# Kernel optimization log

Measured on AMD Instinct MI355X. Metric: run time of the kernel, lower is better.

## Reference

```python
import jax, jax.numpy as jnp
import numpy as np

EPS = 1e-5

def ln(x, gamma, beta):
    m = jnp.mean(x, axis=-1, keepdims=True)
    std = jnp.sqrt(jnp.var(x, axis=-1, keepdims=True) + EPS)
    return gamma * ((x - m) / (std + EPS)) + beta

def hard_sigmoid(x):
    return jnp.clip(0.2 * x + 0.5, 0.0, 1.0)

def setup_inputs() -> dict:
    key = jax.random.key(0)
    B, T, D, U, UEP = 64, 2048, 256, 256, 64
    ks = jax.random.split(key, 16)
    def gn(k, shape, s=0.05):
        return (jax.random.normal(k, shape, dtype=jnp.float32) * s)
    inp = {}
    inp['x'] = jax.random.normal(ks[0], (B, T, D), dtype=jnp.float32)
    inp['mask'] = jax.random.randint(ks[1], (B, T), 0, 2, dtype=jnp.int32)
    inp['W'] = gn(ks[2], (D, 3 * U))
    inp['U'] = gn(ks[3], (U, 3 * U))
    inp['b'] = jnp.zeros((3 * U,), jnp.float32)
    inp['gammas'] = 1.0 + gn(ks[4], (2, 3 * U), 0.1)
    inp['betas'] = gn(ks[5], (2, 3 * U), 0.1)
    inp['W_EP'] = gn(ks[6], (D, 3 * UEP))
    inp['U_EP'] = gn(ks[7], (UEP, 3 * UEP))
    inp['b_EP'] = jnp.zeros((3 * UEP,), jnp.float32)
    inp['gammas_EP'] = 1.0 + gn(ks[8], (2, 3 * UEP), 0.1)
    inp['betas_EP'] = gn(ks[9], (2, 3 * UEP), 0.1)
    inp['W1_EP'] = gn(ks[10], (UEP, 1))
    inp['b1_EP'] = jnp.zeros((1,), jnp.float32)
    return inp

def _gru_step(s1, h_tm1, Umat, g1, bt1, dim):
    # s1: precomputed ln(x@W + b)  [B, 3*dim]
    s2 = ln(h_tm1 @ Umat[:, :2 * dim], g1[:2 * dim], bt1[:2 * dim])
    s = hard_sigmoid(s1[:, :2 * dim] + s2)
    z, r = s[:, :dim], s[:, dim:2 * dim]
    hh = ln((r * h_tm1) @ Umat[:, 2 * dim:], g1[2 * dim:], bt1[2 * dim:])
    return z * h_tm1 + (1.0 - z) * jnp.tanh(s1[:, 2 * dim:] + hh)

def _encoder(x, mask, W, U, b, gammas, betas, W_EP, U_EP, b_EP, gammas_EP, betas_EP, W1_EP, b1_EP):
    B, T, D = x.shape
    dim = U.shape[0]
    dim_ep = U_EP.shape[0]
    # input projections + their LayerNorms depend only on x -> precompute (same math)
    s1_all = ln(jnp.einsum('btd,dk->btk', x, W) + b, gammas[0], betas[0])          # [B,T,3U]
    s1_ep_all = ln(jnp.einsum('btd,dk->btk', x, W_EP) + b_EP, gammas_EP[0], betas_EP[0])  # [B,T,3Uep]
    s1_all = jnp.swapaxes(s1_all, 0, 1)        # [T,B,3U]
    s1_ep_all = jnp.swapaxes(s1_ep_all, 0, 1)  # [T,B,3Uep]
    xm_all = (mask > 0).T                      # [T,B] bool

    def step(carry, inp):
        h_tm1, hep_tm1, is_end_tm1 = carry
        s1, s1e, xm = inp
        h_tm1 = jnp.where(is_end_tm1[:, None] > 0.5, 0.0, h_tm1)
        h = _gru_step(s1, h_tm1, U, gammas[1], betas[1], dim)
        h = jnp.where(xm[:, None], h, h_tm1)
        hep = _gru_step(s1e, hep_tm1, U_EP, gammas_EP[1], betas_EP[1], dim_ep)
        hep = jnp.where(xm[:, None], hep, hep_tm1)
        is_end = jnp.round(jax.nn.sigmoid(hep_tm1 @ W1_EP + b1_EP))[:, 0]
        return (h, hep, is_end), (h, is_end)

    init = (jnp.zeros((B, dim), x.dtype), jnp.zeros((B, dim_ep), x.dtype), jnp.zeros((B,), x.dtype))
    _, (h_seq, end_seq) = jax.lax.scan(step, init, (s1_all, s1_ep_all, xm_all))
    return jnp.swapaxes(h_seq, 0, 1), jnp.swapaxes(end_seq, 0, 1)  # [B,T,U], [B,T]

def reference(x, mask, W, U, b, gammas, betas, W_EP, U_EP, b_EP, gammas_EP, betas_EP, W1_EP, b1_EP):
    return _encoder(x, mask, W, U, b, gammas, betas, W_EP, U_EP, b_EP, gammas_EP, betas_EP, W1_EP, b1_EP)
```

## Files before the change

### kernel.cpp

```cpp
#include <hip/hip_runtime.h>


typedef _Float16 h2  __attribute__((ext_vector_type(2)));
typedef _Float16 v8h __attribute__((ext_vector_type(8)));

__device__ __forceinline__ float fdot2_(h2 a, h2 b, float c) {
#if __has_builtin(__builtin_amdgcn_fdot2)
  return __builtin_amdgcn_fdot2(a, b, c, false);
#else
  return c + (float)a[0] * (float)b[0] + (float)a[1] * (float)b[1];
#endif
}

template <int I>
__device__ __forceinline__ h2 pr(v8h v) {
  h2 r; r[0] = v[2 * I]; r[1] = v[2 * I + 1]; return r;
}

__device__ __forceinline__ void wg_barrier() {
  __builtin_amdgcn_sched_barrier(0);
  asm volatile("s_waitcnt lgkmcnt(0)" ::: "memory");
  __builtin_amdgcn_sched_barrier(0);
  __builtin_amdgcn_s_barrier();
  __builtin_amdgcn_sched_barrier(0);
}

__global__ __launch_bounds__(256) void prep_kernel(
    const float* __restrict__ W, const float* __restrict__ U,
    const float* __restrict__ W_EP,
    _Float16* __restrict__ wt, _Float16* __restrict__ uzr,
    _Float16* __restrict__ uh, float* __restrict__ wept)
{
  const int blk = blockIdx.x;
  const int k = threadIdx.x;
  if (blk < 768) {
    const int j = blk;
    wt[(size_t)j * 256 + k] = (_Float16)W[(size_t)k * 768 + j];
  } else if (blk < 1280) {
    const int j = blk - 768;
    uzr[(size_t)j * 256 + k] = (_Float16)U[(size_t)k * 768 + j];
  } else if (blk < 1536) {
    const int j = blk - 1280;
    const int p = k >> 3, e = k & 7;
    uh[((size_t)p * 256 + j) * 8 + e] = (_Float16)U[(size_t)k * 768 + 512 + j];
  } else {
    const int j = blk - 1536;
    wept[(size_t)j * 256 + k] = W_EP[(size_t)k * 192 + j];
  }
}

__global__ __launch_bounds__(256) void ph1_main_kernel(
    const float* __restrict__ x, const _Float16* __restrict__ wt,
    const float* __restrict__ bvec, const float* __restrict__ gam,
    const float* __restrict__ bet, _Float16* __restrict__ s1out)
{
  __shared__ __align__(16) _Float16 xs[16][256];
  __shared__ float sp[16][768];
  const int tid = threadIdx.x;
  const size_t row0 = (size_t)blockIdx.x * 16;

  #pragma unroll
  for (int i = 0; i < 16; ++i)
    xs[i][tid] = (_Float16)x[(row0 + i) * 256 + tid];
  __syncthreads();

  #pragma unroll 1
  for (int cc = 0; cc < 3; ++cc) {
    const int col = cc * 256 + tid;
    const v8h* wp = (const v8h*)(wt + (size_t)col * 256);
    float acc[16];
    #pragma unroll
    for (int r = 0; r < 16; ++r) acc[r] = 0.f;
    #pragma unroll 4
    for (int c = 0; c < 32; ++c) {
      const v8h w8 = wp[c];
      #pragma unroll
      for (int r = 0; r < 16; ++r) {
        const v8h x8 = *(const v8h*)(&xs[r][c * 8]);
        acc[r] = fdot2_(pr<0>(x8), pr<0>(w8), acc[r]);
        acc[r] = fdot2_(pr<1>(x8), pr<1>(w8), acc[r]);
        acc[r] = fdot2_(pr<2>(x8), pr<2>(w8), acc[r]);
        acc[r] = fdot2_(pr<3>(x8), pr<3>(w8), acc[r]);
      }
    }
    const float bb = bvec[col];
    #pragma unroll
    for (int r = 0; r < 16; ++r) sp[r][col] = acc[r] + bb;
  }
  __syncthreads();

  const int w = tid >> 6, lane = tid & 63;
  for (int rr = 0; rr < 4; ++rr) {
    const int r = (w << 2) | rr;
    float vals[12], sum = 0.f, sq = 0.f;
    #pragma unroll
    for (int j = 0; j < 12; ++j) {
      const float v = sp[r][lane + (j << 6)];
      vals[j] = v; sum += v; sq += v * v;
    }
    #pragma unroll
    for (int m = 32; m >= 1; m >>= 1) {
      sum += __shfl_xor(sum, m); sq += __shfl_xor(sq, m);
    }
    const float mean = sum * (1.f / 768.f);
    const float var = sq * (1.f / 768.f) - mean * mean;
    const float inv = 1.f / (sqrtf(var + 1e-5f) + 1e-5f);
    #pragma unroll
    for (int j = 0; j < 12; ++j) {
      const int c = lane + (j << 6);
      s1out[(row0 + r) * 768 + c] =
          (_Float16)(gam[c] * ((vals[j] - mean) * inv) + bet[c]);
    }
  }
}

__global__ __launch_bounds__(192) void ph1_ep_kernel(
    const float* __restrict__ x, const float* __restrict__ wept,
    const float* __restrict__ bvec, const float* __restrict__ gam,
    const float* __restrict__ bet, void* __restrict__ s1e, const int store64)
{
  __shared__ __align__(16) float xs[16][256];
  __shared__ double sp[16][192];
  const int tid = threadIdx.x;
  const size_t row0 = (size_t)blockIdx.x * 16;

  for (int idx = tid; idx < 4096; idx += 192)
    xs[idx >> 8][idx & 255] = x[row0 * 256 + idx];
  __syncthreads();

  {
    const float4* wp = (const float4*)(wept + (size_t)tid * 256);
    double acc[16];
    #pragma unroll
    for (int r = 0; r < 16; ++r) acc[r] = 0.0;
    #pragma unroll 2
    for (int c = 0; c < 64; ++c) {
      const float4 w4 = wp[c];
      #pragma unroll
      for (int r = 0; r < 16; ++r) {
        const float4 x4 = *(const float4*)(&xs[r][c * 4]);
        acc[r] += (double)x4.x * (double)w4.x;
        acc[r] += (double)x4.y * (double)w4.y;
        acc[r] += (double)x4.z * (double)w4.z;
        acc[r] += (double)x4.w * (double)w4.w;
      }
    }
    const double bb = (double)bvec[tid];
    #pragma unroll
    for (int r = 0; r < 16; ++r) sp[r][tid] = acc[r] + bb;
  }
  __syncthreads();

  const int w = tid >> 6, lane = tid & 63;
  for (int r = w; r < 16; r += 3) {
    double vals[3], sum = 0.0, sq = 0.0;
    #pragma unroll
    for (int j = 0; j < 3; ++j) {
      const double v = sp[r][lane + (j << 6)];
      vals[j] = v; sum += v; sq += v * v;
    }
    #pragma unroll
    for (int m = 32; m >= 1; m >>= 1) {
      sum += __shfl_xor(sum, m); sq += __shfl_xor(sq, m);
    }
    const double mean = sum * (1.0 / 192.0);
    const double var = sq * (1.0 / 192.0) - mean * mean;
    const double den = sqrt(var + 1e-5) + 1e-5;
    #pragma unroll
    for (int j = 0; j < 3; ++j) {
      const int c = lane + (j << 6);
      const double vv = (double)gam[c] * ((vals[j] - mean) / den) + (double)bet[c];
      if (store64) ((double*)s1e)[(row0 + r) * 192 + c] = vv;
      else         ((float*)s1e)[(row0 + r) * 192 + c] = (float)vv;
    }
  }
}

#define OFF_UH     0
#define OFF_MASK   131072
#define OFF_HEP    139264
#define OFF_ZEE    139776
#define OFF_RHEP   140288
#define OFF_EPZRP  140800
#define OFF_EPHHP  140928
#define OFF_H2     140992
#define OFF_RH     141504
#define OFF_HF     142016
#define OFF_Z      143040
#define OFF_ZRP    144064
#define OFF_HHP    144128
#define OFF_FLAG   144160
#define SCAN_LDS_BYTES 144192

__global__ __launch_bounds__(512, 2) void scan_kernel(
    const _Float16* __restrict__ uzr_g, const _Float16* __restrict__ uh_g,
    const float* __restrict__ U_EP, const _Float16* __restrict__ s1,
    const void* __restrict__ s1e_v, const int s1e64,
    const int* __restrict__ mask,
    const float* __restrict__ gam1, const float* __restrict__ bet1,
    const float* __restrict__ gamep1, const float* __restrict__ betep1,
    const float* __restrict__ W1, const float* __restrict__ b1,
    float* __restrict__ out)
{
  extern __shared__ char sm[];
  const int t = threadIdx.x;
  const int b = blockIdx.x;
  const int w = t >> 6;
  const int je  = t >> 2;
  const int qe  = t & 3;
  const int jeh = (t & 255) >> 2;

  float*  hf    = (float*)(sm + OFF_HF);
  float*  flagp = (float*)(sm + OFF_FLAG);
  double* hepd  = (double*)(sm + OFF_HEP);
  int*    maskl = (int*)(sm + OFF_MASK);

  {
    const v8h* src = (const v8h*)uh_g;
    v8h* dst = (v8h*)(sm + OFF_UH);
    #pragma unroll
    for (int i = 0; i < 16; ++i) dst[i * 512 + t] = src[i * 512 + t];
  }
  #pragma unroll
  for (int i = 0; i < 4; ++i) maskl[i * 512 + t] = mask[((size_t)b << 11) + i * 512 + t];

  v8h uzrv[32];
  {
    const v8h* up = (const v8h*)uzr_g + (size_t)t * 32;
    #pragma unroll
    for (int c = 0; c < 32; ++c) uzrv[c] = up[c];
  }
  float uez[16], ueh[16];
  #pragma unroll
  for (int i = 0; i < 16; ++i) uez[i] = U_EP[(size_t)(16 * qe + i) * 192 + je];
  #pragma unroll
  for (int i = 0; i < 16; ++i) ueh[i] = U_EP[(size_t)(16 * qe + i) * 192 + 128 + jeh];

  const float gz = gam1[t],                bz = bet1[t];
  const float gh = gam1[512 + (t & 255)],  bh = bet1[512 + (t & 255)];
  const float gse = gamep1[je],            bse = betep1[je];
  const float ghe = gamep1[128 + jeh],     bhe = betep1[128 + jeh];
  const double w1d = (double)W1[t & 63];
  const double b1d = (double)b1[0];
  const double* dptr = (const double*)s1e_v;
  const float*  fptr = (const float*)s1e_v;

  if (t < 128) { h2 z2; z2[0] = (_Float16)0.f; z2[1] = (_Float16)0.f;
                 ((h2*)(sm + OFF_H2))[t] = z2; }
  if (t < 256) hf[t] = 0.f;
  if (t < 64)  hepd[t] = 0.0;
  if (t < 2)   flagp[t] = 0.f;

  const size_t n0 = (size_t)b << 11;
  float  s1zr_c = (float)s1[n0 * 768 + t];
  float  s1h_c  = (float)s1[n0 * 768 + 512 + (t & 255)];
  double s1ezr_c = s1e64 ? dptr[n0 * 192 + je]
                         : (double)fptr[n0 * 192 + je];
  double s1ehh_c = s1e64 ? dptr[n0 * 192 + 128 + jeh]
                         : (double)fptr[n0 * 192 + 128 + jeh];
  __syncthreads();

  for (int tt = 0; tt < 2048; ++tt) {
    const size_t n = ((size_t)b << 11) | (size_t)tt;
    const float fz = (flagp[tt & 1] > 0.5f) ? 0.f : 1.f;

    if (tt > 0 && t < 256) out[(n - 1) * 256 + t] = hf[t];

    const int ttn = (tt < 2047) ? tt + 1 : 2047;
    const size_t np1 = ((size_t)b << 11) | (size_t)ttn;
    const float  s1zr_n = (float)s1[np1 * 768 + t];
    const float  s1h_n  = (float)s1[np1 * 768 + 512 + (t & 255)];
    const double s1ezr_n = s1e64 ? dptr[np1 * 192 + je]
                                 : (double)fptr[np1 * 192 + je];
    const double s1ehh_n = s1e64 ? dptr[np1 * 192 + 128 + jeh]
                                 : (double)fptr[np1 * 192 + 128 + jeh];

    if (w == 7) {
      double p = hepd[t & 63] * w1d;
      #pragma unroll
      for (int m = 1; m <= 32; m <<= 1) p += __shfl_xor(p, m);
      if (t == 448) {
        const float e = ((p + b1d) > 0.0) ? 1.f : 0.f;
        flagp[(tt + 1) & 1] = e;
        out[(size_t)33554432 + n] = e;
      }
    }

    float d;
    {
      const v8h* hv = (const v8h*)(sm + OFF_H2);
      float a0 = 0.f, a1 = 0.f, a2 = 0.f, a3 = 0.f;
      #pragma unroll
      for (int c = 0; c < 32; ++c) {
        const v8h hc = hv[c];
        a0 = fdot2_(pr<0>(hc), pr<0>(uzrv[c]), a0);
        a1 = fdot2_(pr<1>(hc), pr<1>(uzrv[c]), a1);
        a2 = fdot2_(pr<2>(hc), pr<2>(uzrv[c]), a2);
        a3 = fdot2_(pr<3>(hc), pr<3>(uzrv[c]), a3);
      }
      d = ((a0 + a1) + (a2 + a3)) * fz;
      float s_ = d, q_ = d * d;
      #pragma unroll
      for (int m = 1; m <= 32; m <<= 1) { s_ += __shfl_xor(s_, m); q_ += __shfl_xor(q_, m); }
      if ((t & 63) == 0) ((float2*)(sm + OFF_ZRP))[w] = make_float2(s_, q_);
    }
    double de;
    {
      const double2* hp = (const double2*)(hepd + 16 * qe);
      double acc = 0.0;
      #pragma unroll
      for (int i = 0; i < 8; ++i) {
        const double2 hv2 = hp[i];
        acc += hv2.x * (double)uez[2 * i] + hv2.y * (double)uez[2 * i + 1];
      }
      acc += __shfl_xor(acc, 1); acc += __shfl_xor(acc, 2);
      de = acc;
      double es = de, eq = de * de;
      #pragma unroll
      for (int m = 4; m <= 32; m <<= 1) { es += __shfl_xor(es, m); eq += __shfl_xor(eq, m); }
      if ((t & 63) == 0) ((double2*)(sm + OFF_EPZRP))[w] = make_double2(es, eq);
    }
    wg_barrier();

    {
      float S = 0.f, Q = 0.f;
      const float4* zp = (const float4*)(sm + OFF_ZRP);
      #pragma unroll
      for (int i = 0; i < 4; ++i) { const float4 v = zp[i]; S += v.x + v.z; Q += v.y + v.w; }
      const float mean = S * (1.f / 512.f);
      const float var = Q * (1.f / 512.f) - mean * mean;
      const float inv = 1.f / (sqrtf(var + 1e-5f) + 1e-5f);
      const float s2v = gz * ((d - mean) * inv) + bz;
      float sv = 0.2f * (s1zr_c + s2v) + 0.5f;
      sv = fminf(fmaxf(sv, 0.f), 1.f);
      if (t < 256) ((float*)(sm + OFF_Z))[t] = sv;
      else {
        const float rhv = sv * (fz * hf[t - 256]);
        ((_Float16*)(sm + OFF_RH))[t - 256] = (_Float16)rhv;
      }
    }
    if ((t & 3) == 0) {
      double S = 0.0, Q = 0.0;
      const double2* ep = (const double2*)(sm + OFF_EPZRP);
      #pragma unroll
      for (int i = 0; i < 8; ++i) { S += ep[i].x; Q += ep[i].y; }
      const double mean = S * (1.0 / 128.0);
      const double var = Q * (1.0 / 128.0) - mean * mean;
      const double den = sqrt(var + 1e-5) + 1e-5;
      const double s2e = (double)gse * ((de - mean) / den) + (double)bse;
      double se = 0.2 * (s1ezr_c + s2e) + 0.5;
      se = fmin(fmax(se, 0.0), 1.0);
      if (je < 64) ((double*)(sm + OFF_ZEE))[je] = se;
      else         ((double*)(sm + OFF_RHEP))[je - 64] = se * hepd[je - 64];
    }
    wg_barrier();

    float dh = 0.f;
    double deh = 0.0;
    if (t < 256) {
      const v8h* rhv8 = (const v8h*)(sm + OFF_RH);
      const v8h* uhv  = (const v8h*)(sm + OFF_UH);
      float c0 = 0.f, c1 = 0.f, c2 = 0.f, c3 = 0.f;
      #pragma unroll
      for (int p = 0; p < 32; ++p) {
        const v8h rc = rhv8[p];
        const v8h uc = uhv[p * 256 + t];
        c0 = fdot2_(pr<0>(rc), pr<0>(uc), c0);
        c1 = fdot2_(pr<1>(rc), pr<1>(uc), c1);
        c2 = fdot2_(pr<2>(rc), pr<2>(uc), c2);
        c3 = fdot2_(pr<3>(rc), pr<3>(uc), c3);
      }
      dh = (c0 + c1) + (c2 + c3);
      float s_ = dh, q_ = dh * dh;
      #pragma unroll
      for (int m = 1; m <= 32; m <<= 1) { s_ += __shfl_xor(s_, m); q_ += __shfl_xor(q_, m); }
      if ((t & 63) == 0) ((float2*)(sm + OFF_HHP))[w] = make_float2(s_, q_);
    } else {
      const double2* rp = (const double2*)((double*)(sm + OFF_RHEP) + 16 * qe);
      double acc = 0.0;
      #pragma unroll
      for (int i = 0; i < 8; ++i) {
        const double2 rv = rp[i];
        acc += rv.x * (double)ueh[2 * i] + rv.y * (double)ueh[2 * i + 1];
      }
      acc += __shfl_xor(acc, 1); acc += __shfl_xor(acc, 2);
      deh = acc;
      double es = deh, eq = deh * deh;
      #pragma unroll
      for (int m = 4; m <= 32; m <<= 1) { es += __shfl_xor(es, m); eq += __shfl_xor(eq, m); }
      if ((t & 63) == 0) ((double2*)(sm + OFF_EPHHP))[w - 4] = make_double2(es, eq);
    }
    wg_barrier();

    const int xm = maskl[tt];
    if (t < 256) {
      float S = 0.f, Q = 0.f;
      const float4* hp4 = (const float4*)(sm + OFF_HHP);
      #pragma unroll
      for (int i = 0; i < 2; ++i) { const float4 v = hp4[i]; S += v.x + v.z; Q += v.y + v.w; }
      const float mean = S * (1.f / 256.f);
      const float var = Q * (1.f / 256.f) - mean * mean;
      const float inv = 1.f / (sqrtf(var + 1e-5f) + 1e-5f);
      const float hhv = gh * ((dh - mean) * inv) + bh;
      const float z = ((float*)(sm + OFF_Z))[t];
      const float hzf = fz * hf[t];
      const float hn = z * hzf + (1.f - z) * tanhf(s1h_c + hhv);
      const float hc_ = (xm > 0) ? hn : hzf;
      hf[t] = hc_;
      const float ho = __shfl_xor(hc_, 1);
      if (!(t & 1)) {
        h2 p2; p2[0] = (_Float16)hc_; p2[1] = (_Float16)ho;
        ((h2*)(sm + OFF_H2))[t >> 1] = p2;
      }
    } else if ((t & 3) == 0) {
      double S = 0.0, Q = 0.0;
      const double2* ep = (const double2*)(sm + OFF_EPHHP);
      #pragma unroll
      for (int i = 0; i < 4; ++i) { S += ep[i].x; Q += ep[i].y; }
      const double mean = S * (1.0 / 64.0);
      const double var = Q * (1.0 / 64.0) - mean * mean;
      const double den = sqrt(var + 1e-5) + 1e-5;
      const double hhe = (double)ghe * ((deh - mean) / den) + (double)bhe;
      const double ze = ((double*)(sm + OFF_ZEE))[jeh];
      const double hold = hepd[jeh];
      const double hepn = ze * hold + (1.0 - ze) * tanh(s1ehh_c + hhe);
      hepd[jeh] = (xm > 0) ? hepn : hold;
    }
    wg_barrier();

    s1zr_c = s1zr_n; s1h_c = s1h_n; s1ezr_c = s1ezr_n; s1ehh_c = s1ehh_n;
  }
  if (t < 256) out[((((size_t)b << 11) | 2047)) * 256 + t] = hf[t];
}

extern "C" void kernel_launch(void* const* d_in, const int* in_sizes, int n_in,
                              void* d_out, int out_size, void* d_ws, size_t ws_size,
                              hipStream_t stream)
{
  (void)in_sizes; (void)n_in; (void)out_size;
  const float* x       = (const float*)d_in[0];
  const int*   mask    = (const int*)d_in[1];
  const float* W       = (const float*)d_in[2];
  const float* U       = (const float*)d_in[3];
  const float* bvec    = (const float*)d_in[4];
  const float* gammas  = (const float*)d_in[5];
  const float* betas   = (const float*)d_in[6];
  const float* W_EP    = (const float*)d_in[7];
  const float* U_EP    = (const float*)d_in[8];
  const float* b_EP    = (const float*)d_in[9];
  const float* gammasE = (const float*)d_in[10];
  const float* betasE  = (const float*)d_in[11];
  const float* W1_EP   = (const float*)d_in[12];
  const float* b1_EP   = (const float*)d_in[13];
  float* out = (float*)d_out;

  const size_t NR = 131072;
  const size_t S1_SZ    = NR * 768 * 2;
  const size_t S1E64_SZ = NR * 192 * 8;
  const size_t S1E32_SZ = NR * 192 * 4;
  const size_t WSMALL = 262144 + 131072 + 393216 + 196608;
  const int s1e64 = (ws_size >= S1_SZ + S1E64_SZ + WSMALL) ? 1 : 0;
  const size_t S1E_SZ = s1e64 ? S1E64_SZ : S1E32_SZ;
  if (ws_size < S1_SZ + S1E32_SZ + WSMALL) return;

  char* ws = (char*)d_ws;
  size_t off = 0;
  void* s1e      = (void*)(ws + off);      off += S1E_SZ;
  _Float16* s1   = (_Float16*)(ws + off);  off += S1_SZ;
  _Float16* uzr  = (_Float16*)(ws + off);  off += 262144;
  _Float16* uh   = (_Float16*)(ws + off);  off += 131072;
  _Float16* wt   = (_Float16*)(ws + off);  off += 393216;
  float* wept    = (float*)(ws + off);     off += 196608;

  prep_kernel<<<dim3(1728), dim3(256), 0, stream>>>(
      W, U, W_EP, wt, uzr, uh, wept);
  ph1_main_kernel<<<dim3(8192), dim3(256), 0, stream>>>(
      x, wt, bvec, gammas, betas, s1);
  ph1_ep_kernel<<<dim3(8192), dim3(192), 0, stream>>>(
      x, wept, b_EP, gammasE, betasE, s1e, s1e64);

  hipFuncSetAttribute(reinterpret_cast<const void*>(scan_kernel),
                      hipFuncAttributeMaxDynamicSharedMemorySize, SCAN_LDS_BYTES);
  scan_kernel<<<dim3(64), dim3(512), SCAN_LDS_BYTES, stream>>>(
      uzr, uh, U_EP, s1, (const void*)s1e, s1e64, mask,
      gammas + 768, betas + 768, gammasE + 192, betasE + 192,
      W1_EP, b1_EP, out);
}
```

Baseline: 20.75 ms.

## Split EP GRU recurrence into separate single-wave scan kernel feeding reset flags

```diff
diff --git a/kernel.cpp b/kernel.cpp
--- a/kernel.cpp
+++ b/kernel.cpp
@@ -15,6 +15,14 @@
 template <int I>
 __device__ __forceinline__ h2 pr(v8h v) {
   h2 r; r[0] = v[2 * I]; r[1] = v[2 * I + 1]; return r;
+}
+
+__device__ __forceinline__ double bcast_d(double v, int k) {
+  const int2 p = __builtin_bit_cast(int2, v);
+  int2 q;
+  q.x = __builtin_amdgcn_readlane(p.x, k);
+  q.y = __builtin_amdgcn_readlane(p.y, k);
+  return __builtin_bit_cast(double, q);
 }
 
 __device__ __forceinline__ void wg_barrier() {
@@ -38,7 +46,8 @@
     wt[(size_t)j * 256 + k] = (_Float16)W[(size_t)k * 768 + j];
   } else if (blk < 1280) {
     const int j = blk - 768;
-    uzr[(size_t)j * 256 + k] = (_Float16)U[(size_t)k * 768 + j];
+    const int c = k >> 3, e = k & 7;
+    uzr[((size_t)c * 512 + j) * 8 + e] = (_Float16)U[(size_t)k * 768 + j];
   } else if (blk < 1536) {
     const int j = blk - 1280;
     const int p = k >> 3, e = k & 7;
@@ -176,190 +185,211 @@
   }
 }
 
-#define OFF_UH     0
-#define OFF_MASK   131072
-#define OFF_HEP    139264
-#define OFF_ZEE    139776
-#define OFF_RHEP   140288
-#define OFF_EPZRP  140800
-#define OFF_EPHHP  140928
-#define OFF_H2     140992
-#define OFF_RH     141504
-#define OFF_HF     142016
-#define OFF_Z      143040
-#define OFF_ZRP    144064
-#define OFF_HHP    144128
-#define OFF_FLAG   144160
-#define SCAN_LDS_BYTES 144192
-
-__global__ __launch_bounds__(512, 2) void scan_kernel(
-    const _Float16* __restrict__ uzr_g, const _Float16* __restrict__ uh_g,
-    const float* __restrict__ U_EP, const _Float16* __restrict__ s1,
-    const void* __restrict__ s1e_v, const int s1e64,
-    const int* __restrict__ mask,
-    const float* __restrict__ gam1, const float* __restrict__ bet1,
+__global__ __launch_bounds__(64) void ep_scan_kernel(
+    const float* __restrict__ U_EP, const void* __restrict__ s1e_v,
+    const int s1e64, const int* __restrict__ mask,
     const float* __restrict__ gamep1, const float* __restrict__ betep1,
     const float* __restrict__ W1, const float* __restrict__ b1,
+    float* __restrict__ out, float* __restrict__ fzw)
+{
+  const int l = threadIdx.x;
+  const int b = blockIdx.x;
+
+  float uezA[64], uezB[64], uehh[64];
+  #pragma unroll
+  for (int k = 0; k < 64; ++k) uezA[k] = U_EP[(size_t)k * 192 + l];
+  #pragma unroll
+  for (int k = 0; k < 64; ++k) uezB[k] = U_EP[(size_t)k * 192 + 64 + l];
+  #pragma unroll
+  for (int k = 0; k < 64; ++k) uehh[k] = U_EP[(size_t)k * 192 + 128 + l];
+
+  const double gseA = (double)gamep1[l],       bseA = (double)betep1[l];
+  const double gseB = (double)gamep1[64 + l],  bseB = (double)betep1[64 + l];
+  const double ghe  = (double)gamep1[128 + l], bhe  = (double)betep1[128 + l];
+  const double w1d = (double)W1[l];
+  const double b1d = (double)b1[0];
+  const double* dptr = (const double*)s1e_v;
+  const float*  fptr = (const float*)s1e_v;
+
+  double hep = 0.0;
+  if (l == 0) fzw[(size_t)b * 2048] = 0.f;
+
+  const size_t n0 = (size_t)b << 11;
+  double s1eA_c = s1e64 ? dptr[n0 * 192 + l]       : (double)fptr[n0 * 192 + l];
+  double s1eB_c = s1e64 ? dptr[n0 * 192 + 64 + l]  : (double)fptr[n0 * 192 + 64 + l];
+  double s1eh_c = s1e64 ? dptr[n0 * 192 + 128 + l] : (double)fptr[n0 * 192 + 128 + l];
+  int mask_c = mask[n0];
+
+  for (int tt = 0; tt < 2048; ++tt) {
+    const size_t n = ((size_t)b << 11) | (size_t)tt;
+    const int ttn = (tt < 2047) ? tt + 1 : 2047;
+    const size_t np1 = ((size_t)b << 11) | (size_t)ttn;
+    const double s1eA_n = s1e64 ? dptr[np1 * 192 + l]       : (double)fptr[np1 * 192 + l];
+    const double s1eB_n = s1e64 ? dptr[np1 * 192 + 64 + l]  : (double)fptr[np1 * 192 + 64 + l];
+    const double s1eh_n = s1e64 ? dptr[np1 * 192 + 128 + l] : (double)fptr[np1 * 192 + 128 + l];
+    const int mask_n = mask[np1];
+
+    {
+      double p = hep * w1d;
+      #pragma unroll
+      for (int m = 1; m <= 32; m <<= 1) p += __shfl_xor(p, m);
+      if (l == 0) {
+        const float e = ((p + b1d) > 0.0) ? 1.f : 0.f;
+        if (tt < 2047) fzw[(size_t)b * 2048 + tt + 1] = e;
+        out[(size_t)33554432 + n] = e;
+      }
+    }
+
+    double dA = 0.0, dB = 0.0;
+    #pragma unroll
+    for (int k = 0; k < 64; ++k) {
+      const double hk = bcast_d(hep, k);
+      dA += hk * (double)uezA[k];
+      dB += hk * (double)uezB[k];
+    }
+    {
+      double S = dA + dB, Q = dA * dA + dB * dB;
+      #pragma unroll
+      for (int m = 1; m <= 32; m <<= 1) { S += __shfl_xor(S, m); Q += __shfl_xor(Q, m); }
+      const double mean = S * (1.0 / 128.0);
+      const double var = Q * (1.0 / 128.0) - mean * mean;
+      const double den = sqrt(var + 1e-5) + 1e-5;
+      double seA = 0.2 * (s1eA_c + (gseA * ((dA - mean) / den) + bseA)) + 0.5;
+      seA = fmin(fmax(seA, 0.0), 1.0);
+      double seB = 0.2 * (s1eB_c + (gseB * ((dB - mean) / den) + bseB)) + 0.5;
+      seB = fmin(fmax(seB, 0.0), 1.0);
+      const double rh = seB * hep;
+
+      double dh = 0.0;
+      #pragma unroll
+      for (int k = 0; k < 64; ++k) {
+        const double rk = bcast_d(rh, k);
+        dh += rk * (double)uehh[k];
+      }
+      double S2 = dh, Q2 = dh * dh;
+      #pragma unroll
+      for (int m = 1; m <= 32; m <<= 1) { S2 += __shfl_xor(S2, m); Q2 += __shfl_xor(Q2, m); }
+      const double mean2 = S2 * (1.0 / 64.0);
+      const double var2 = Q2 * (1.0 / 64.0) - mean2 * mean2;
+      const double den2 = sqrt(var2 + 1e-5) + 1e-5;
+      const double hhe = ghe * ((dh - mean2) / den2) + bhe;
+      const double hepn = seA * hep + (1.0 - seA) * tanh(s1eh_c + hhe);
+      hep = (mask_c > 0) ? hepn : hep;
+    }
+
+    s1eA_c = s1eA_n; s1eB_c = s1eB_n; s1eh_c = s1eh_n; mask_c = mask_n;
+  }
+}
+
+#define OFFM_UH   0
+#define OFFM_H2   131072
+#define OFFM_RH   131584
+#define OFFM_HF   132096
+#define OFFM_ZRP  133120
+#define OFFM_HHP  133184
+#define SCANM_LDS_BYTES 133248
+
+__global__ __launch_bounds__(512, 2) void main_scan_kernel(
+    const _Float16* __restrict__ uzr_g, const _Float16* __restrict__ uh_g,
+    const _Float16* __restrict__ s1, const int* __restrict__ mask,
+    const float* __restrict__ fzw,
+    const float* __restrict__ gam1, const float* __restrict__ bet1,
     float* __restrict__ out)
 {
   extern __shared__ char sm[];
   const int t = threadIdx.x;
   const int b = blockIdx.x;
   const int w = t >> 6;
-  const int je  = t >> 2;
-  const int qe  = t & 3;
-  const int jeh = (t & 255) >> 2;
-
-  float*  hf    = (float*)(sm + OFF_HF);
-  float*  flagp = (float*)(sm + OFF_FLAG);
-  double* hepd  = (double*)(sm + OFF_HEP);
-  int*    maskl = (int*)(sm + OFF_MASK);
+
+  float* hf = (float*)(sm + OFFM_HF);
 
   {
     const v8h* src = (const v8h*)uh_g;
-    v8h* dst = (v8h*)(sm + OFF_UH);
+    v8h* dst = (v8h*)(sm + OFFM_UH);
     #pragma unroll
     for (int i = 0; i < 16; ++i) dst[i * 512 + t] = src[i * 512 + t];
   }
-  #pragma unroll
-  for (int i = 0; i < 4; ++i) maskl[i * 512 + t] = mask[((size_t)b << 11) + i * 512 + t];
-
-  v8h uzrv[32];
-  {
-    const v8h* up = (const v8h*)uzr_g + (size_t)t * 32;
-    #pragma unroll
-    for (int c = 0; c < 32; ++c) uzrv[c] = up[c];
-  }
-  float uez[16], ueh[16];
-  #pragma unroll
-  for (int i = 0; i < 16; ++i) uez[i] = U_EP[(size_t)(16 * qe + i) * 192 + je];
-  #pragma unroll
-  for (int i = 0; i < 16; ++i) ueh[i] = U_EP[(size_t)(16 * qe + i) * 192 + 128 + jeh];
-
-  const float gz = gam1[t],                bz = bet1[t];
-  const float gh = gam1[512 + (t & 255)],  bh = bet1[512 + (t & 255)];
-  const float gse = gamep1[je],            bse = betep1[je];
-  const float ghe = gamep1[128 + jeh],     bhe = betep1[128 + jeh];
-  const double w1d = (double)W1[t & 63];
-  const double b1d = (double)b1[0];
-  const double* dptr = (const double*)s1e_v;
-  const float*  fptr = (const float*)s1e_v;
+
+  const float gz = gam1[t], bz = bet1[t];
+  const float gh = (t < 256) ? gam1[512 + t] : 0.f;
+  const float bh = (t < 256) ? bet1[512 + t] : 0.f;
 
   if (t < 128) { h2 z2; z2[0] = (_Float16)0.f; z2[1] = (_Float16)0.f;
-                 ((h2*)(sm + OFF_H2))[t] = z2; }
+                 ((h2*)(sm + OFFM_H2))[t] = z2; }
   if (t < 256) hf[t] = 0.f;
-  if (t < 64)  hepd[t] = 0.0;
-  if (t < 2)   flagp[t] = 0.f;
 
   const size_t n0 = (size_t)b << 11;
-  float  s1zr_c = (float)s1[n0 * 768 + t];
-  float  s1h_c  = (float)s1[n0 * 768 + 512 + (t & 255)];
-  double s1ezr_c = s1e64 ? dptr[n0 * 192 + je]
-                         : (double)fptr[n0 * 192 + je];
-  double s1ehh_c = s1e64 ? dptr[n0 * 192 + 128 + jeh]
-                         : (double)fptr[n0 * 192 + 128 + jeh];
+  float s1z_c = (float)s1[n0 * 768 + t];
+  float s1h_c = (t < 256) ? (float)s1[n0 * 768 + 512 + t] : 0.f;
+  float fz_c = fzw[(size_t)b * 2048];
+  int   xm_c = mask[n0];
   __syncthreads();
 
   for (int tt = 0; tt < 2048; ++tt) {
     const size_t n = ((size_t)b << 11) | (size_t)tt;
-    const float fz = (flagp[tt & 1] > 0.5f) ? 0.f : 1.f;
+    const float fz = (fz_c > 0.5f) ? 0.f : 1.f;
+    const int xm = xm_c;
 
     if (tt > 0 && t < 256) out[(n - 1) * 256 + t] = hf[t];
 
     const int ttn = (tt < 2047) ? tt + 1 : 2047;
     const size_t np1 = ((size_t)b << 11) | (size_t)ttn;
-    const float  s1zr_n = (float)s1[np1 * 768 + t];
-    const float  s1h_n  = (float)s1[np1 * 768 + 512 + (t & 255)];
-    const double s1ezr_n = s1e64 ? dptr[np1 * 192 + je]
-                                 : (double)fptr[np1 * 192 + je];
-    const double s1ehh_n = s1e64 ? dptr[np1 * 192 + 128 + jeh]
-                                 : (double)fptr[np1 * 192 + 128 + jeh];
-
-    if (w == 7) {
-      double p = hepd[t & 63] * w1d;
-      #pragma unroll
-      for (int m = 1; m <= 32; m <<= 1) p += __shfl_xor(p, m);
-      if (t == 448) {
-        const float e = ((p + b1d) > 0.0) ? 1.f : 0.f;
-        flagp[(tt + 1) & 1] = e;
-        out[(size_t)33554432 + n] = e;
-      }
-    }
-
-    float d;
+    const float s1z_n = (float)s1[np1 * 768 + t];
+    const float s1h_n = (t < 256) ? (float)s1[np1 * 768 + 512 + t] : 0.f;
+    const float fz_n = fzw[(size_t)b * 2048 + ttn];
+    const int   xm_n = mask[np1];
+
+    const v8h* uzb = (const v8h*)uzr_g;
+    asm volatile("" : "+v"(uzb));
+    v8h wz[8];
+    #pragma unroll
+    for (int q = 0; q < 8; ++q) wz[q] = uzb[(size_t)q * 512 + t];
+
+    const v8h* hv = (const v8h*)(sm + OFFM_H2);
+    float a0 = 0.f, a1 = 0.f, a2 = 0.f, a3 = 0.f;
+    #pragma unroll
+    for (int k = 0; k < 32; ++k) {
+      const v8h hc = hv[k];
+      const v8h wc = wz[k & 7];
+      a0 = fdot2_(pr<0>(hc), pr<0>(wc), a0);
+      a1 = fdot2_(pr<1>(hc), pr<1>(wc), a1);
+      a2 = fdot2_(pr<2>(hc), pr<2>(wc), a2);
+      a3 = fdot2_(pr<3>(hc), pr<3>(wc), a3);
+      if (k < 24) wz[k & 7] = uzb[(size_t)(k + 8) * 512 + t];
+    }
+    const float d = ((a0 + a1) + (a2 + a3)) * fz;
     {
-      const v8h* hv = (const v8h*)(sm + OFF_H2);
-      float a0 = 0.f, a1 = 0.f, a2 = 0.f, a3 = 0.f;
-      #pragma unroll
-      for (int c = 0; c < 32; ++c) {
-        const v8h hc = hv[c];
-        a0 = fdot2_(pr<0>(hc), pr<0>(uzrv[c]), a0);
-        a1 = fdot2_(pr<1>(hc), pr<1>(uzrv[c]), a1);
-        a2 = fdot2_(pr<2>(hc), pr<2>(uzrv[c]), a2);
-        a3 = fdot2_(pr<3>(hc), pr<3>(uzrv[c]), a3);
-      }
-      d = ((a0 + a1) + (a2 + a3)) * fz;
       float s_ = d, q_ = d * d;
       #pragma unroll
       for (int m = 1; m <= 32; m <<= 1) { s_ += __shfl_xor(s_, m); q_ += __shfl_xor(q_, m); }
-      if ((t & 63) == 0) ((float2*)(sm + OFF_ZRP))[w] = make_float2(s_, q_);
-    }
-    double de;
-    {
-      const double2* hp = (const double2*)(hepd + 16 * qe);
-      double acc = 0.0;
-      #pragma unroll
-      for (int i = 0; i < 8; ++i) {
-        const double2 hv2 = hp[i];
-        acc += hv2.x * (double)uez[2 * i] + hv2.y * (double)uez[2 * i + 1];
-      }
-      acc += __shfl_xor(acc, 1); acc += __shfl_xor(acc, 2);
-      de = acc;
-      double es = de, eq = de * de;
-      #pragma unroll
-      for (int m = 4; m <= 32; m <<= 1) { es += __shfl_xor(es, m); eq += __shfl_xor(eq, m); }
-      if ((t & 63) == 0) ((double2*)(sm + OFF_EPZRP))[w] = make_double2(es, eq);
+      if ((t & 63) == 0) ((float2*)(sm + OFFM_ZRP))[w] = make_float2(s_, q_);
     }
     wg_barrier();
 
+    float zreg = 0.f;
     {
       float S = 0.f, Q = 0.f;
-      const float4* zp = (const float4*)(sm + OFF_ZRP);
+      const float4* zp = (const float4*)(sm + OFFM_ZRP);
       #pragma unroll
       for (int i = 0; i < 4; ++i) { const float4 v = zp[i]; S += v.x + v.z; Q += v.y + v.w; }
       const float mean = S * (1.f / 512.f);
       const float var = Q * (1.f / 512.f) - mean * mean;
       const float inv = 1.f / (sqrtf(var + 1e-5f) + 1e-5f);
       const float s2v = gz * ((d - mean) * inv) + bz;
-      float sv = 0.2f * (s1zr_c + s2v) + 0.5f;
+      float sv = 0.2f * (s1z_c + s2v) + 0.5f;
       sv = fminf(fmaxf(sv, 0.f), 1.f);
-      if (t < 256) ((float*)(sm + OFF_Z))[t] = sv;
+      if (t < 256) zreg = sv;
       else {
         const float rhv = sv * (fz * hf[t - 256]);
-        ((_Float16*)(sm + OFF_RH))[t - 256] = (_Float16)rhv;
-      }
-    }
-    if ((t & 3) == 0) {
-      double S = 0.0, Q = 0.0;
-      const double2* ep = (const double2*)(sm + OFF_EPZRP);
-      #pragma unroll
-      for (int i = 0; i < 8; ++i) { S += ep[i].x; Q += ep[i].y; }
-      const double mean = S * (1.0 / 128.0);
-      const double var = Q * (1.0 / 128.0) - mean * mean;
-      const double den = sqrt(var + 1e-5) + 1e-5;
-      const double s2e = (double)gse * ((de - mean) / den) + (double)bse;
-      double se = 0.2 * (s1ezr_c + s2e) + 0.5;
-      se = fmin(fmax(se, 0.0), 1.0);
-      if (je < 64) ((double*)(sm + OFF_ZEE))[je] = se;
-      else         ((double*)(sm + OFF_RHEP))[je - 64] = se * hepd[je - 64];
+        ((_Float16*)(sm + OFFM_RH))[t - 256] = (_Float16)rhv;
+      }
     }
     wg_barrier();
 
     float dh = 0.f;
-    double deh = 0.0;
     if (t < 256) {
-      const v8h* rhv8 = (const v8h*)(sm + OFF_RH);
-      const v8h* uhv  = (const v8h*)(sm + OFF_UH);
+      const v8h* rhv8 = (const v8h*)(sm + OFFM_RH);
+      const v8h* uhv  = (const v8h*)(sm + OFFM_UH);
       float c0 = 0.f, c1 = 0.f, c2 = 0.f, c3 = 0.f;
       #pragma unroll
       for (int p = 0; p < 32; ++p) {
@@ -374,61 +404,32 @@
       float s_ = dh, q_ = dh * dh;
       #pragma unroll
       for (int m = 1; m <= 32; m <<= 1) { s_ += __shfl_xor(s_, m); q_ += __shfl_xor(q_, m); }
-      if ((t & 63) == 0) ((float2*)(sm + OFF_HHP))[w] = make_float2(s_, q_);
-    } else {
-      const double2* rp = (const double2*)((double*)(sm + OFF_RHEP) + 16 * qe);
-      double acc = 0.0;
-      #pragma unroll
-      for (int i = 0; i < 8; ++i) {
-        const double2 rv = rp[i];
-        acc += rv.x * (double)ueh[2 * i] + rv.y * (double)ueh[2 * i + 1];
-      }
-      acc += __shfl_xor(acc, 1); acc += __shfl_xor(acc, 2);
-      deh = acc;
-      double es = deh, eq = deh * deh;
-      #pragma unroll
-      for (int m = 4; m <= 32; m <<= 1) { es += __shfl_xor(es, m); eq += __shfl_xor(eq, m); }
-      if ((t & 63) == 0) ((double2*)(sm + OFF_EPHHP))[w - 4] = make_double2(es, eq);
+      if ((t & 63) == 0) ((float2*)(sm + OFFM_HHP))[w] = make_float2(s_, q_);
     }
     wg_barrier();
 
-    const int xm = maskl[tt];
     if (t < 256) {
       float S = 0.f, Q = 0.f;
-      const float4* hp4 = (const float4*)(sm + OFF_HHP);
+      const float4* hp4 = (const float4*)(sm + OFFM_HHP);
       #pragma unroll
       for (int i = 0; i < 2; ++i) { const float4 v = hp4[i]; S += v.x + v.z; Q += v.y + v.w; }
       const float mean = S * (1.f / 256.f);
       const float var = Q * (1.f / 256.f) - mean * mean;
       const float inv = 1.f / (sqrtf(var + 1e-5f) + 1e-5f);
       const float hhv = gh * ((dh - mean) * inv) + bh;
-      const float z = ((float*)(sm + OFF_Z))[t];
-      const float hzf = fz * hf[t];
-      const float hn = z * hzf + (1.f - z) * tanhf(s1h_c + hhv);
-      const float hc_ = (xm > 0) ? hn : hzf;
-      hf[t] = hc_;
-      const float ho = __shfl_xor(hc_, 1);
+      const float hz = fz * hf[t];
+      const float hn = zreg * hz + (1.f - zreg) * tanhf(s1h_c + hhv);
+      const float hc = (xm > 0) ? hn : hz;
+      hf[t] = hc;
+      const float ho = __shfl_xor(hc, 1);
       if (!(t & 1)) {
-        h2 p2; p2[0] = (_Float16)hc_; p2[1] = (_Float16)ho;
-        ((h2*)(sm + OFF_H2))[t >> 1] = p2;
-      }
-    } else if ((t & 3) == 0) {
-      double S = 0.0, Q = 0.0;
-      const double2* ep = (const double2*)(sm + OFF_EPHHP);
-      #pragma unroll
-      for (int i = 0; i < 4; ++i) { S += ep[i].x; Q += ep[i].y; }
-      const double mean = S * (1.0 / 64.0);
-      const double var = Q * (1.0 / 64.0) - mean * mean;
-      const double den = sqrt(var + 1e-5) + 1e-5;
-      const double hhe = (double)ghe * ((deh - mean) / den) + (double)bhe;
-      const double ze = ((double*)(sm + OFF_ZEE))[jeh];
-      const double hold = hepd[jeh];
-      const double hepn = ze * hold + (1.0 - ze) * tanh(s1ehh_c + hhe);
-      hepd[jeh] = (xm > 0) ? hepn : hold;
+        h2 p2; p2[0] = (_Float16)hc; p2[1] = (_Float16)ho;
+        ((h2*)(sm + OFFM_H2))[t >> 1] = p2;
+      }
     }
     wg_barrier();
 
-    s1zr_c = s1zr_n; s1h_c = s1h_n; s1ezr_c = s1ezr_n; s1ehh_c = s1ehh_n;
+    s1z_c = s1z_n; s1h_c = s1h_n; fz_c = fz_n; xm_c = xm_n;
   }
   if (t < 256) out[((((size_t)b << 11) | 2047)) * 256 + t] = hf[t];
 }
@@ -458,7 +459,7 @@
   const size_t S1_SZ    = NR * 768 * 2;
   const size_t S1E64_SZ = NR * 192 * 8;
   const size_t S1E32_SZ = NR * 192 * 4;
-  const size_t WSMALL = 262144 + 131072 + 393216 + 196608;
+  const size_t WSMALL = 262144 + 131072 + 393216 + 196608 + 524288;
   const int s1e64 = (ws_size >= S1_SZ + S1E64_SZ + WSMALL) ? 1 : 0;
   const size_t S1E_SZ = s1e64 ? S1E64_SZ : S1E32_SZ;
   if (ws_size < S1_SZ + S1E32_SZ + WSMALL) return;
@@ -471,18 +472,20 @@
   _Float16* uh   = (_Float16*)(ws + off);  off += 131072;
   _Float16* wt   = (_Float16*)(ws + off);  off += 393216;
   float* wept    = (float*)(ws + off);     off += 196608;
+  float* fzw     = (float*)(ws + off);     off += 524288;
 
   prep_kernel<<<dim3(1728), dim3(256), 0, stream>>>(
       W, U, W_EP, wt, uzr, uh, wept);
+  ph1_ep_kernel<<<dim3(8192), dim3(192), 0, stream>>>(
+      x, wept, b_EP, gammasE, betasE, s1e, s1e64);
+  ep_scan_kernel<<<dim3(64), dim3(64), 0, stream>>>(
+      U_EP, (const void*)s1e, s1e64, mask,
+      gammasE + 192, betasE + 192, W1_EP, b1_EP, out, fzw);
   ph1_main_kernel<<<dim3(8192), dim3(256), 0, stream>>>(
       x, wt, bvec, gammas, betas, s1);
-  ph1_ep_kernel<<<dim3(8192), dim3(192), 0, stream>>>(
-      x, wept, b_EP, gammasE, betasE, s1e, s1e64);
-
-  hipFuncSetAttribute(reinterpret_cast<const void*>(scan_kernel),
-                      hipFuncAttributeMaxDynamicSharedMemorySize, SCAN_LDS_BYTES);
-  scan_kernel<<<dim3(64), dim3(512), SCAN_LDS_BYTES, stream>>>(
-      uzr, uh, U_EP, s1, (const void*)s1e, s1e64, mask,
-      gammas + 768, betas + 768, gammasE + 192, betasE + 192,
-      W1_EP, b1_EP, out);
-}
+
+  hipFuncSetAttribute(reinterpret_cast<const void*>(main_scan_kernel),
+                      hipFuncAttributeMaxDynamicSharedMemorySize, SCANM_LDS_BYTES);
+  main_scan_kernel<<<dim3(64), dim3(512), SCANM_LDS_BYTES, stream>>>(
+      uzr, uh, s1, mask, fzw, gammas + 768, betas + 768, out);
+}
```

New measurement: 16.70 ms. 19.5% less time.
